# Kernel tuning notes

Measured on AMD Instinct MI355X. Metric: run time of the kernel, lower is better.

The kernel has to match this reference:

```python
import jax, jax.numpy as jnp
import numpy as np

B, N, C = 16, 4096, 512
FR = 2          # fr_ratio
NH = 8          # num_heads
CF = C // FR    # 256, q/k/v projection dim
HD = (C // NH) // FR  # 32, per-head dim after fr reduction
EPS = 1e-4


def _abs_clamp(t):
    # sign(t) * clamp(|t|, 1e-4, 1e4), as in the torch module's abs_clamp
    return jnp.sign(t) * jnp.clip(jnp.abs(t), 1e-4, 1e4)


def setup_inputs() -> dict:
    key = jax.random.key(0)
    ks = jax.random.split(key, 8)
    s = 0.02  # trunc_normal_(std=0.02) init scale
    return {
        "query": jax.random.normal(ks[0], (B, N, C), jnp.float32),
        "Wq": jax.random.normal(ks[1], (CF, C), jnp.float32) * s,
        "bq": jnp.zeros((CF,), jnp.float32),
        "Wk": jax.random.normal(ks[2], (CF, C), jnp.float32) * s,
        "bk": jnp.zeros((CF,), jnp.float32),
        "Wv": jax.random.normal(ks[3], (CF, C), jnp.float32) * s,
        "bv": jnp.zeros((CF,), jnp.float32),
        "Wo": jax.random.normal(ks[4], (C, CF), jnp.float32) * s,
        "bo": jnp.zeros((C,), jnp.float32),
        "Wse1": jax.random.normal(ks[5], (C // 2, C), jnp.float32) * s,
        "Wse2": jax.random.normal(ks[6], (C, C // 2), jnp.float32) * s,
        "H": 64,
        "W": 64,
    }


def reference(query, Wq, bq, Wk, bk, Wv, bv, Wo, bo, Wse1, Wse2, H, W):
    Bq, Nq, Cq = query.shape  # N == H*W
    # --- squeeze-excitation gate: mean over tokens -> 2-layer MLP -> sigmoid
    se = jnp.mean(query, axis=1)                                   # [B, C]
    se = jax.nn.sigmoid(jax.nn.relu(se @ Wse1.T) @ Wse2.T)         # [B, C]

    # --- q/k/v projections (sr_ratio=1: k/v from full-length query)
    q = jax.nn.relu(query @ Wq.T + bq).reshape(Bq, Nq, NH, HD)     # [B,N,h,d]
    k = jax.nn.relu(query @ Wk.T + bk).reshape(Bq, Nq, NH, HD)
    v = (query @ Wv.T + bv).reshape(Bq, Nq, NH, HD)

    # --- cosFormer-style 2D positional feature maps
    c = jnp.pi / 2
    idx = jnp.arange(Nq)
    a = (c * (idx // W).astype(query.dtype) / H)[None, :, None, None]  # row angle
    b = (c * (idx % W).astype(query.dtype) / W)[None, :, None, None]   # col angle
    q_ = jnp.concatenate([q * jnp.cos(a), q * jnp.sin(a),
                          q * jnp.cos(b), q * jnp.sin(b)], axis=-1)    # [B,N,h,4d]
    k_ = jnp.concatenate([k * jnp.cos(a), k * jnp.sin(a),
                          k * jnp.cos(b), k * jnp.sin(b)], axis=-1)    # sr_ratio=1 -> same angles

    # --- linear attention: kv state then q lookup, with abs-clamping
    kv = _abs_clamp(jnp.einsum('bnhf,bnhd->bhfd', k_, v))          # [B,h,4d,d]
    k_sum = jnp.sum(k_, axis=1, keepdims=True)                     # [B,1,h,4d]
    z = _abs_clamp(1.0 / (jnp.sum(q_ * k_sum, axis=-1) + EPS))     # [B,N,h]
    out = _abs_clamp(jnp.einsum('bnhf,bhfd->bnhd', q_, kv))        # [B,N,h,d]
    out = _abs_clamp(out * z[..., None])

    # --- output projection + SE residual gating
    out = _abs_clamp(out.reshape(Bq, Nq, CF) @ Wo.T + bo)          # [B,N,C]
    out = _abs_clamp(out + out * se[:, None, :])
    return out
```

## Files before the change

kernel.cpp:

```cpp
#include <hip/hip_runtime.h>
#include <math.h>

#define B_   16
#define N_   4096
#define C_   512
#define CF_  256
#define NH_  8
#define HD_  32
#define FHD_ 128
#define BN_  (B_ * N_)
#define EPS_ 1e-4f
#define PI2F 1.5707963267948966f

typedef _Float16 half8 __attribute__((ext_vector_type(8)));
typedef _Float16 half4 __attribute__((ext_vector_type(4)));
typedef _Float16 half2v __attribute__((ext_vector_type(2)));
typedef float f32x4 __attribute__((ext_vector_type(4)));
typedef unsigned short u16x8 __attribute__((ext_vector_type(8)));

__device__ __forceinline__ float abs_clamp(float t) {
    float a = fminf(fmaxf(fabsf(t), 1e-4f), 1e4f);
    return t > 0.f ? a : (t < 0.f ? -a : 0.f);
}
__device__ __forceinline__ void gld16(const void* g, void* l) {
    __builtin_amdgcn_global_load_lds(
        (const __attribute__((address_space(1))) void*)g,
        (__attribute__((address_space(3))) void*)l, 16, 0, 0);
}

__global__ __launch_bounds__(256) void se_sum_kernel(const float* __restrict__ q,
                                                     float* __restrict__ sesum,
                                                     _Float16* __restrict__ q16) {
    int b = blockIdx.x, chunk = blockIdx.y;
    int t = threadIdx.x;
    int c0 = 2 * t;
    const float* p = q + ((size_t)b * N_ + (size_t)chunk * 256) * C_ + c0;
    _Float16* o = q16 + ((size_t)b * N_ + (size_t)chunk * 256) * C_ + c0;
    float a0 = 0.f, a1 = 0.f;
    for (int n = 0; n < 256; n++) {
        float2 v = *(const float2*)(p + (size_t)n * C_);
        a0 += v.x;
        a1 += v.y;
        half2v hv;
        hv[0] = (_Float16)v.x;
        hv[1] = (_Float16)v.y;
        *(half2v*)(o + (size_t)n * C_) = hv;
    }
    atomicAdd(&sesum[b * C_ + c0], a0);
    atomicAdd(&sesum[b * C_ + c0 + 1], a1);
}

__global__ __launch_bounds__(256) void se_gate_kernel(const float* __restrict__ sesum,
                                                      const float* __restrict__ Wse1,
                                                      const float* __restrict__ Wse2,
                                                      float* __restrict__ segate) {
    __shared__ float sm[C_];
    __shared__ float hm[C_ / 2];
    int b = blockIdx.x, t = threadIdx.x;
    sm[t]       = sesum[b * C_ + t]       * (1.f / N_);
    sm[t + 256] = sesum[b * C_ + t + 256] * (1.f / N_);
    __syncthreads();
    {
        const float* w = Wse1 + (size_t)t * C_;
        float acc = 0.f;
        for (int c2 = 0; c2 < C_; c2++) acc += sm[c2] * w[c2];
        hm[t] = fmaxf(acc, 0.f);
    }
    __syncthreads();
    for (int r = 0; r < 2; r++) {
        int c2 = t + r * 256;
        const float* w2 = Wse2 + (size_t)c2 * (C_ / 2);
        float a2 = 0.f;
        for (int j = 0; j < C_ / 2; j++) a2 += hm[j] * w2[j];
        segate[b * C_ + c2] = 1.f / (1.f + expf(-a2));
    }
}

__global__ __launch_bounds__(256) void convert_w(const float* __restrict__ Wq,
                                                 const float* __restrict__ Wk,
                                                 const float* __restrict__ Wv,
                                                 const float* __restrict__ Wo,
                                                 _Float16* __restrict__ wcat,
                                                 _Float16* __restrict__ wo16) {
    int i = blockIdx.x * 256 + threadIdx.x;
    if (i < 768 * 512) {
        int r = i >> 9, c = i & 511;
        float w = (r < 256) ? Wq[(size_t)r * 512 + c]
                : (r < 512) ? Wk[(size_t)(r - 256) * 512 + c]
                            : Wv[(size_t)(r - 512) * 512 + c];
        wcat[i] = (_Float16)w;
    } else {
        int j = i - 768 * 512;
        wo16[j] = (_Float16)Wo[j];
    }
}

__global__ __launch_bounds__(256) void gemm_qkv(
    const _Float16* __restrict__ A16, const _Float16* __restrict__ Bw,
    const float* __restrict__ bq, const float* __restrict__ bk, const float* __restrict__ bv,
    _Float16* __restrict__ Oq, _Float16* __restrict__ kT, _Float16* __restrict__ vT) {
    constexpr int K = 512;
    constexpr int NITER = K / 32;

    __shared__ __align__(16) unsigned short As[2][128 * 32];
    __shared__ __align__(16) unsigned short Bs[2][128 * 32];

    const int t = threadIdx.x;
    const int did = blockIdx.x + 6 * blockIdx.y;
    const int lid = (did & 7) * 384 + (did >> 3);
    const int bx = lid % 6;
    const int Mb = (lid / 6) * 128;
    const int nrow0 = bx * 128;

    const int lane = t & 63;
    const int wv = t >> 6;
    const int mq = (wv >> 1) * 64;
    const int nq = (wv & 1) * 64;
    const int mrow = lane & 15;
    const int kq = lane >> 4;
    const int fragoff = mrow * 32 + ((kq ^ ((mrow >> 1) & 3)) * 8);

    const unsigned char *asrc0, *asrc1, *bsrc0, *bsrc1;
    int off0, off1;
    {
        int cid0 = t, cid1 = t + 256;
        int m0 = cid0 >> 2, c0 = (cid0 & 3) ^ ((m0 >> 1) & 3);
        int m1 = cid1 >> 2, c1 = (cid1 & 3) ^ ((m1 >> 1) & 3);
        asrc0 = (const unsigned char*)(A16 + (size_t)(Mb + m0) * K + c0 * 8);
        asrc1 = (const unsigned char*)(A16 + (size_t)(Mb + m1) * K + c1 * 8);
        bsrc0 = (const unsigned char*)(Bw + (size_t)(nrow0 + m0) * K + c0 * 8);
        bsrc1 = (const unsigned char*)(Bw + (size_t)(nrow0 + m1) * K + c1 * 8);
        off0 = cid0 * 8;
        off1 = cid1 * 8;
    }

    f32x4 acc[4][4];
#pragma unroll
    for (int mi = 0; mi < 4; mi++)
#pragma unroll
        for (int ni = 0; ni < 4; ni++) acc[mi][ni] = (f32x4){0.f, 0.f, 0.f, 0.f};

    gld16(asrc0, &As[0][off0]);
    gld16(asrc1, &As[0][off1]);
    gld16(bsrc0, &Bs[0][off0]);
    gld16(bsrc1, &Bs[0][off1]);
    __syncthreads();

    int cur = 0;
#pragma unroll 1
    for (int it = 0; it < NITER; ++it) {
        if (it + 1 < NITER) {
            gld16(asrc0 + (it + 1) * 64, &As[cur ^ 1][off0]);
            gld16(asrc1 + (it + 1) * 64, &As[cur ^ 1][off1]);
            gld16(bsrc0 + (it + 1) * 64, &Bs[cur ^ 1][off0]);
            gld16(bsrc1 + (it + 1) * 64, &Bs[cur ^ 1][off1]);
        }

        half8 ah[4], bh[4];
#pragma unroll
        for (int mi = 0; mi < 4; mi++)
            ah[mi] = *(const half8*)&As[cur][(mq + mi * 16) * 32 + fragoff];
#pragma unroll
        for (int ni = 0; ni < 4; ni++)
            bh[ni] = *(const half8*)&Bs[cur][(nq + ni * 16) * 32 + fragoff];
#pragma unroll
        for (int mi = 0; mi < 4; mi++)
#pragma unroll
            for (int ni = 0; ni < 4; ni++)
                acc[mi][ni] = __builtin_amdgcn_mfma_f32_16x16x32_f16(ah[mi], bh[ni], acc[mi][ni], 0, 0, 0);

        if (it + 1 < NITER) __syncthreads();
        cur ^= 1;
    }

#pragma unroll
    for (int ni = 0; ni < 4; ni++) {
        int gc = nrow0 + nq + ni * 16 + mrow;
        int mat = gc >> 8;
        int col = gc & 255;
        float bb = (mat == 0 ? bq : mat == 1 ? bk : bv)[col];
        if (mat == 0) {
#pragma unroll
            for (int mi = 0; mi < 4; mi++)
#pragma unroll
                for (int r = 0; r < 4; r++) {
                    int m = Mb + mq + mi * 16 + kq * 4 + r;
                    float v2 = fmaxf(acc[mi][ni][r] + bb, 0.f);
                    Oq[(size_t)m * CF_ + col] = (_Float16)v2;
                }
        } else {
            _Float16* OT = (mat == 1) ? kT : vT;
#pragma unroll
            for (int mi = 0; mi < 4; mi++) {
                int m0r = Mb + mq + mi * 16 + kq * 4;
                half4 hv;
#pragma unroll
                for (int r = 0; r < 4; r++) {
                    float v2 = acc[mi][ni][r] + bb;
                    if (mat == 1) v2 = fmaxf(v2, 0.f);
                    hv[r] = (_Float16)v2;
                }
                *(half4*)&OT[(size_t)col * BN_ + m0r] = hv;
            }
        }
    }
}

__global__ __launch_bounds__(256) void gemm_out(
    const _Float16* __restrict__ A16, const _Float16* __restrict__ Bw,
    const float* __restrict__ bo, const float* __restrict__ sg,
    float* __restrict__ Of) {
    constexpr int K = 256;
    constexpr int NITER = K / 32;

    __shared__ __align__(16) unsigned short As[2][128 * 32];
    __shared__ __align__(16) unsigned short Bs[2][128 * 32];

    const int t = threadIdx.x;
    const int did = blockIdx.x + 4 * blockIdx.y;
    const int lid = (did & 7) * 256 + (did >> 3);
    const int bx = lid & 3;
    const int Mb = (lid >> 2) * 128;
    const int nrow0 = bx * 128;

    const int lane = t & 63;
    const int wv = t >> 6;
    const int mq = (wv >> 1) * 64;
    const int nq = (wv & 1) * 64;
    const int mrow = lane & 15;
    const int kq = lane >> 4;
    const int fragoff = mrow * 32 + ((kq ^ ((mrow >> 1) & 3)) * 8);

    const unsigned char *asrc0, *asrc1, *bsrc0, *bsrc1;
    int off0, off1;
    {
        int cid0 = t, cid1 = t + 256;
        int m0 = cid0 >> 2, c0 = (cid0 & 3) ^ ((m0 >> 1) & 3);
        int m1 = cid1 >> 2, c1 = (cid1 & 3) ^ ((m1 >> 1) & 3);
        asrc0 = (const unsigned char*)(A16 + (size_t)(Mb + m0) * K + c0 * 8);
        asrc1 = (const unsigned char*)(A16 + (size_t)(Mb + m1) * K + c1 * 8);
        bsrc0 = (const unsigned char*)(Bw + (size_t)(nrow0 + m0) * K + c0 * 8);
        bsrc1 = (const unsigned char*)(Bw + (size_t)(nrow0 + m1) * K + c1 * 8);
        off0 = cid0 * 8;
        off1 = cid1 * 8;
    }

    f32x4 acc[4][4];
#pragma unroll
    for (int mi = 0; mi < 4; mi++)
#pragma unroll
        for (int ni = 0; ni < 4; ni++) acc[mi][ni] = (f32x4){0.f, 0.f, 0.f, 0.f};

    gld16(asrc0, &As[0][off0]);
    gld16(asrc1, &As[0][off1]);
    gld16(bsrc0, &Bs[0][off0]);
    gld16(bsrc1, &Bs[0][off1]);
    __syncthreads();

    int cur = 0;
#pragma unroll 1
    for (int it = 0; it < NITER; ++it) {
        if (it + 1 < NITER) {
            gld16(asrc0 + (it + 1) * 64, &As[cur ^ 1][off0]);
            gld16(asrc1 + (it + 1) * 64, &As[cur ^ 1][off1]);
            gld16(bsrc0 + (it + 1) * 64, &Bs[cur ^ 1][off0]);
            gld16(bsrc1 + (it + 1) * 64, &Bs[cur ^ 1][off1]);
        }

        half8 ah[4], bh[4];
#pragma unroll
        for (int mi = 0; mi < 4; mi++)
            ah[mi] = *(const half8*)&As[cur][(mq + mi * 16) * 32 + fragoff];
#pragma unroll
        for (int ni = 0; ni < 4; ni++)
            bh[ni] = *(const half8*)&Bs[cur][(nq + ni * 16) * 32 + fragoff];
#pragma unroll
        for (int mi = 0; mi < 4; mi++)
#pragma unroll
            for (int ni = 0; ni < 4; ni++)
                acc[mi][ni] = __builtin_amdgcn_mfma_f32_16x16x32_f16(ah[mi], bh[ni], acc[mi][ni], 0, 0, 0);

        if (it + 1 < NITER) __syncthreads();
        cur ^= 1;
    }

    int b = Mb >> 12;
#pragma unroll
    for (int ni = 0; ni < 4; ni++) {
        int gc = nrow0 + nq + ni * 16 + mrow;
        float bb = bo[gc];
        float gv = sg[b * C_ + gc];
#pragma unroll
        for (int mi = 0; mi < 4; mi++)
#pragma unroll
            for (int r = 0; r < 4; r++) {
                int m = Mb + mq + mi * 16 + kq * 4 + r;
                float v2 = abs_clamp(acc[mi][ni][r] + bb);
                v2 = abs_clamp(v2 * (1.f + gv));
                Of[(size_t)m * C_ + gc] = v2;
            }
    }
}

__global__ __launch_bounds__(256) void kv_mfma_kernel(const _Float16* __restrict__ kin,
                                                      const _Float16* __restrict__ vin,
                                                      float* __restrict__ kvout,
                                                      float* __restrict__ ksum) {
    __shared__ __align__(16) unsigned short Ah[128 * 64];
    __shared__ __align__(16) unsigned short Bh[48 * 64];

    const int t = threadIdx.x;
    const int c8 = blockIdx.x;
    const int h = blockIdx.y, b = blockIdx.z;
    const int dp = t & 31;
    const int octet = t >> 5;

    if (t < 128) {
        int r = 32 + (t & 15);
        int oc = t >> 4;
        int off = r * 64 + (((oc ^ ((r >> 3) & 7)) & 7) * 8);
        unsigned short fill = (r == 32) ? (unsigned short)0x3C00 : (unsigned short)0;
        u16x8 z = {fill, fill, fill, fill, fill, fill, fill, fill};
        *(u16x8*)&Bh[off] = z;
    }

    float cbv[8], sbv[8];
#pragma unroll
    for (int i = 0; i < 8; i++) {
        float ang = (PI2F / 64.f) * (float)(octet * 8 + i);
        cbv[i] = cosf(ang);
        sbv[i] = sinf(ang);
    }

    const int lane = t & 63;
    const int wv = t >> 6;
    const int mrow = lane & 15;
    const int kq = lane >> 4;

    f32x4 acc[2][3];
#pragma unroll
    for (int mi = 0; mi < 2; mi++)
#pragma unroll
        for (int ni = 0; ni < 3; ni++) acc[mi][ni] = (f32x4){0.f, 0.f, 0.f, 0.f};

    int offA[4];
#pragma unroll
    for (int tvar = 0; tvar < 4; tvar++) {
        int f = tvar * 32 + dp;
        offA[tvar] = f * 64 + (((octet ^ ((f >> 3) & 7)) & 7) * 8);
    }
    const int offB = dp * 64 + (((octet ^ ((dp >> 3) & 7)) & 7) * 8);

    const size_t colbase = (size_t)(h * HD_ + dp) * BN_ + (size_t)b * N_;

#pragma unroll 1
    for (int ch = 0; ch < 8; ch++) {
        const int n0 = c8 * 512 + ch * 64;
        const int rrow = n0 >> 6;
        float aang = (PI2F / 64.f) * (float)rrow;
        float ca = cosf(aang), sa = sinf(aang);

        half8 k8 = *(const half8*)(kin + colbase + n0 + octet * 8);
        half8 v8 = *(const half8*)(vin + colbase + n0 + octet * 8);
        float kvl[8];
#pragma unroll
        for (int i = 0; i < 8; i++) kvl[i] = (float)k8[i];

        __syncthreads();

#pragma unroll
        for (int tvar = 0; tvar < 4; tvar++) {
            half8 hv;
#pragma unroll
            for (int i = 0; i < 8; i++) {
                float val = kvl[i] * (tvar == 0 ? ca : tvar == 1 ? sa : tvar == 2 ? cbv[i] : sbv[i]);
                hv[i] = (_Float16)val;
            }
            *(half8*)&Ah[offA[tvar]] = hv;
        }
        *(half8*)&Bh[offB] = v8;
        __syncthreads();

#pragma unroll
        for (int s = 0; s < 2; s++) {
            half8 ah[2], bh[3];
            int koct = s * 4 + kq;
#pragma unroll
            for (int mi = 0; mi < 2; mi++) {
                int f = (wv * 2 + mi) * 16 + mrow;
                ah[mi] = *(const half8*)&Ah[f * 64 + (((koct ^ ((f >> 3) & 7)) & 7) * 8)];
            }
#pragma unroll
            for (int ni = 0; ni < 3; ni++) {
                int nr = ni * 16 + mrow;
                bh[ni] = *(const half8*)&Bh[nr * 64 + (((koct ^ ((nr >> 3) & 7)) & 7) * 8)];
            }
#pragma unroll
            for (int mi = 0; mi < 2; mi++)
#pragma unroll
                for (int ni = 0; ni < 3; ni++)
                    acc[mi][ni] = __builtin_amdgcn_mfma_f32_16x16x32_f16(ah[mi], bh[ni], acc[mi][ni], 0, 0, 0);
        }
    }

    float* kvp = kvout + (size_t)(b * NH_ + h) * FHD_ * HD_;
    float* ksp = ksum + (size_t)(b * NH_ + h) * FHD_;
#pragma unroll
    for (int mi = 0; mi < 2; mi++) {
        int mt = wv * 2 + mi;
#pragma unroll
        for (int r = 0; r < 4; r++) {
            int f = mt * 16 + kq * 4 + r;
            atomicAdd(&kvp[(size_t)mrow * FHD_ + f], acc[mi][0][r]);
            atomicAdd(&kvp[(size_t)(16 + mrow) * FHD_ + f], acc[mi][1][r]);
            if (mrow == 0) atomicAdd(&ksp[f], acc[mi][2][r]);
        }
    }
}

__global__ __launch_bounds__(256) void attn_kernel(const _Float16* __restrict__ qbuf,
                                                   const float* __restrict__ kvin,
                                                   const float* __restrict__ ksum,
                                                   _Float16* __restrict__ ob) {
    __shared__ __align__(16) unsigned short Aq[128 * 128];
    __shared__ __align__(16) unsigned short Bk[48 * 128];
    __shared__ float zS[128];

    const int chunk = blockIdx.x;
    const int h = blockIdx.y, b = blockIdx.z;
    const int t = threadIdx.x;
    const int n0 = chunk * 128;

    {
        const float* kvp = kvin + ((size_t)(b * NH_ + h)) * (HD_ * FHD_);
        int d = t >> 3;
        int c0 = (t & 7) * 2;
#pragma unroll
        for (int cc = 0; cc < 2; cc++) {
            int c = c0 + cc;
            const float* src = kvp + (size_t)d * FHD_ + c * 8;
            half8 hv;
#pragma unroll
            for (int i = 0; i < 8; i++) hv[i] = (_Float16)abs_clamp(src[i]);
            *(half8*)&Bk[d * 128 + ((c ^ (d & 7)) * 8)] = hv;
        }
        if (t < 16) {
            const float* ks = ksum + ((size_t)(b * NH_ + h)) * FHD_ + t * 8;
            half8 hv;
#pragma unroll
            for (int i = 0; i < 8; i++) hv[i] = (_Float16)ks[i];
            *(half8*)&Bk[32 * 128 + (t * 8)] = hv;
        } else {
            int idx = t - 16;
            int r = 33 + (idx >> 4), c = idx & 15;
            half8 z = {};
            *(half8*)&Bk[r * 128 + ((c ^ (r & 7)) * 8)] = z;
        }
    }
    {
        int tok = t >> 1, hf = t & 1;
        int n = n0 + tok;
        const _Float16* qp = qbuf + ((size_t)b * N_ + n) * CF_ + h * HD_;
        half8 q0 = *(const half8*)(qp + 0);
        half8 q1 = *(const half8*)(qp + 8);
        half8 q2 = *(const half8*)(qp + 16);
        half8 q3 = *(const half8*)(qp + 24);
        float f0, f1;
        if (hf == 0) {
            float aa = (PI2F / 64.f) * (float)(n >> 6);
            f0 = cosf(aa); f1 = sinf(aa);
        } else {
            float ab = (PI2F / 64.f) * (float)(n & 63);
            f0 = cosf(ab); f1 = sinf(ab);
        }
#pragma unroll
        for (int ti = 0; ti < 2; ti++) {
            float fac = ti ? f1 : f0;
#pragma unroll
            for (int dc = 0; dc < 4; dc++) {
                half8 qv = (dc == 0) ? q0 : (dc == 1) ? q1 : (dc == 2) ? q2 : q3;
                half8 hv;
#pragma unroll
                for (int i = 0; i < 8; i++) hv[i] = (_Float16)((float)qv[i] * fac);
                int c = hf * 8 + ti * 4 + dc;
                *(half8*)&Aq[tok * 128 + ((c ^ (tok & 7)) * 8)] = hv;
            }
        }
    }
    __syncthreads();

    const int lane = t & 63;
    const int wv = t >> 6;
    const int mrow = lane & 15;
    const int kq = lane >> 4;

    f32x4 acc[2][3];
#pragma unroll
    for (int mi = 0; mi < 2; mi++)
#pragma unroll
        for (int ni = 0; ni < 3; ni++) acc[mi][ni] = (f32x4){0.f, 0.f, 0.f, 0.f};

#pragma unroll
    for (int ks = 0; ks < 4; ks++) {
        half8 ah[2], bh[3];
        int cpos = ks * 4 + kq;
#pragma unroll
        for (int mi = 0; mi < 2; mi++) {
            int row = wv * 32 + mi * 16 + mrow;
            ah[mi] = *(const half8*)&Aq[row * 128 + ((cpos ^ (row & 7)) * 8)];
        }
#pragma unroll
        for (int ni = 0; ni < 3; ni++) {
            int row = ni * 16 + mrow;
            bh[ni] = *(const half8*)&Bk[row * 128 + ((cpos ^ (row & 7)) * 8)];
        }
#pragma unroll
        for (int mi = 0; mi < 2; mi++)
#pragma unroll
            for (int ni = 0; ni < 3; ni++)
                acc[mi][ni] = __builtin_amdgcn_mfma_f32_16x16x32_f16(ah[mi], bh[ni], acc[mi][ni], 0, 0, 0);
    }

    if (mrow == 0) {
#pragma unroll
        for (int mi = 0; mi < 2; mi++)
#pragma unroll
            for (int r = 0; r < 4; r++)
                zS[wv * 32 + mi * 16 + kq * 4 + r] = acc[mi][2][r];
    }
    __syncthreads();

#pragma unroll
    for (int mi = 0; mi < 2; mi++) {
#pragma unroll
        for (int r = 0; r < 4; r++) {
            int tok = wv * 32 + mi * 16 + kq * 4 + r;
            float z = abs_clamp(1.f / (zS[tok] + EPS_));
            float v0 = abs_clamp(abs_clamp(acc[mi][0][r]) * z);
            float v1 = abs_clamp(abs_clamp(acc[mi][1][r]) * z);
            size_t base = ((size_t)b * N_ + n0 + tok) * CF_ + h * HD_;
            ob[base + mrow] = (_Float16)v0;
            ob[base + 16 + mrow] = (_Float16)v1;
        }
    }
}

extern "C" void kernel_launch(void* const* d_in, const int* in_sizes, int n_in,
                              void* d_out, int out_size, void* d_ws, size_t ws_size,
                              hipStream_t stream) {
    (void)in_sizes; (void)n_in; (void)out_size; (void)ws_size;
    const float* query = (const float*)d_in[0];
    const float* Wq = (const float*)d_in[1];
    const float* bq = (const float*)d_in[2];
    const float* Wk = (const float*)d_in[3];
    const float* bk = (const float*)d_in[4];
    const float* Wv = (const float*)d_in[5];
    const float* bv = (const float*)d_in[6];
    const float* Wo = (const float*)d_in[7];
    const float* bo = (const float*)d_in[8];
    const float* Wse1 = (const float*)d_in[9];
    const float* Wse2 = (const float*)d_in[10];
    float* out = (float*)d_out;

    unsigned char* ws = (unsigned char*)d_ws;
    const size_t MB = 1024ull * 1024ull;
    _Float16* q16 = (_Float16*)(ws + 0);
    _Float16* ob  = (_Float16*)(ws + 0);
    _Float16* qb  = (_Float16*)(ws + 64 * MB);
    _Float16* kbT = (_Float16*)(ws + 96 * MB);
    _Float16* vbT = (_Float16*)(ws + 128 * MB);
    _Float16* wcat = (_Float16*)(ws + 160 * MB);
    _Float16* wo16 = (_Float16*)(ws + 160 * MB + 786432);
    float* kvb = (float*)(ws + 161 * MB);
    float* ksb = (float*)(ws + 163 * MB);
    float* ssb = (float*)(ws + 163 * MB + 65536);
    float* sgb = (float*)(ws + 163 * MB + 98304);

    hipMemsetAsync(kvb, 0, 2097152 + 65536 + 32768, stream);

    convert_w<<<2048, 256, 0, stream>>>(Wq, Wk, Wv, Wo, wcat, wo16);
    se_sum_kernel<<<dim3(B_, 16), 256, 0, stream>>>(query, ssb, q16);
    se_gate_kernel<<<B_, 256, 0, stream>>>(ssb, Wse1, Wse2, sgb);
    gemm_qkv<<<dim3(6, 512), 256, 0, stream>>>(q16, wcat, bq, bk, bv, qb, kbT, vbT);
    kv_mfma_kernel<<<dim3(8, NH_, B_), 256, 0, stream>>>(kbT, vbT, kvb, ksb);
    attn_kernel<<<dim3(32, NH_, B_), 256, 0, stream>>>(qb, kvb, ksb, ob);
    gemm_out<<<dim3(4, 512), 256, 0, stream>>>(ob, wo16, bo, sgb, out);
}
```

Measured before the change: 509.1 us.

## Restructure attention feature maps, widen kv chunks, and vectorize SE reduction

The SE sum/convert kernel now uses float4 loads over 32-token slices, and the grid is four times larger for more parallelism. The kv kernel processes 128 tokens per chunk with a wider LDS tile, halving the number of barrier iterations. The attention kernel stops building the 4x-expanded q feature map in LDS. It instead runs four MFMA passes of raw q against each kv block and combines them with per-token cos/sin factors. This cuts LDS writes and conversion work but increases the accumulator register count, which may reduce occupancy.

```diff
diff --git a/kernel.cpp b/kernel.cpp
--- a/kernel.cpp
+++ b/kernel.cpp
@@ -14,7 +14,6 @@
 
 typedef _Float16 half8 __attribute__((ext_vector_type(8)));
 typedef _Float16 half4 __attribute__((ext_vector_type(4)));
-typedef _Float16 half2v __attribute__((ext_vector_type(2)));
 typedef float f32x4 __attribute__((ext_vector_type(4)));
 typedef unsigned short u16x8 __attribute__((ext_vector_type(8)));
 
@@ -33,21 +32,24 @@
                                                      _Float16* __restrict__ q16) {
     int b = blockIdx.x, chunk = blockIdx.y;
     int t = threadIdx.x;
-    int c0 = 2 * t;
-    const float* p = q + ((size_t)b * N_ + (size_t)chunk * 256) * C_ + c0;
-    _Float16* o = q16 + ((size_t)b * N_ + (size_t)chunk * 256) * C_ + c0;
-    float a0 = 0.f, a1 = 0.f;
-    for (int n = 0; n < 256; n++) {
-        float2 v = *(const float2*)(p + (size_t)n * C_);
-        a0 += v.x;
-        a1 += v.y;
-        half2v hv;
-        hv[0] = (_Float16)v.x;
-        hv[1] = (_Float16)v.y;
-        *(half2v*)(o + (size_t)n * C_) = hv;
-    }
-    atomicAdd(&sesum[b * C_ + c0], a0);
-    atomicAdd(&sesum[b * C_ + c0 + 1], a1);
+    int c = (t & 127) * 4;
+    int tok0 = chunk * 64 + (t >> 7) * 32;
+    const float* p = q + ((size_t)b * N_ + tok0) * C_ + c;
+    _Float16* o = q16 + ((size_t)b * N_ + tok0) * C_ + c;
+    float a0 = 0.f, a1 = 0.f, a2 = 0.f, a3 = 0.f;
+#pragma unroll 4
+    for (int n = 0; n < 32; n++) {
+        float4 v = *(const float4*)(p + (size_t)n * C_);
+        a0 += v.x; a1 += v.y; a2 += v.z; a3 += v.w;
+        half4 hv;
+        hv[0] = (_Float16)v.x; hv[1] = (_Float16)v.y;
+        hv[2] = (_Float16)v.z; hv[3] = (_Float16)v.w;
+        *(half4*)(o + (size_t)n * C_) = hv;
+    }
+    atomicAdd(&sesum[b * C_ + c + 0], a0);
+    atomicAdd(&sesum[b * C_ + c + 1], a1);
+    atomicAdd(&sesum[b * C_ + c + 2], a2);
+    atomicAdd(&sesum[b * C_ + c + 3], a3);
 }
 
 __global__ __launch_bounds__(256) void se_gate_kernel(const float* __restrict__ sesum,
@@ -306,28 +308,27 @@
                                                       const _Float16* __restrict__ vin,
                                                       float* __restrict__ kvout,
                                                       float* __restrict__ ksum) {
-    __shared__ __align__(16) unsigned short Ah[128 * 64];
-    __shared__ __align__(16) unsigned short Bh[48 * 64];
+    __shared__ __align__(16) unsigned short Ah[128 * 128];
+    __shared__ __align__(16) unsigned short Bh[48 * 128];
 
     const int t = threadIdx.x;
     const int c8 = blockIdx.x;
     const int h = blockIdx.y, b = blockIdx.z;
     const int dp = t & 31;
-    const int octet = t >> 5;
-
-    if (t < 128) {
-        int r = 32 + (t & 15);
-        int oc = t >> 4;
-        int off = r * 64 + (((oc ^ ((r >> 3) & 7)) & 7) * 8);
+    const int oct = t >> 5;
+
+    {
+        int r = 32 + (t >> 4);
+        int c = t & 15;
         unsigned short fill = (r == 32) ? (unsigned short)0x3C00 : (unsigned short)0;
         u16x8 z = {fill, fill, fill, fill, fill, fill, fill, fill};
-        *(u16x8*)&Bh[off] = z;
+        *(u16x8*)&Bh[r * 128 + ((c ^ (r & 7)) * 8)] = z;
     }
 
     float cbv[8], sbv[8];
 #pragma unroll
     for (int i = 0; i < 8; i++) {
-        float ang = (PI2F / 64.f) * (float)(octet * 8 + i);
+        float ang = (PI2F / 64.f) * (float)(oct * 8 + i);
         cbv[i] = cosf(ang);
         sbv[i] = sinf(ang);
     }
@@ -343,57 +344,67 @@
 #pragma unroll
         for (int ni = 0; ni < 3; ni++) acc[mi][ni] = (f32x4){0.f, 0.f, 0.f, 0.f};
 
-    int offA[4];
+    int offAa[4], offAb[4];
 #pragma unroll
     for (int tvar = 0; tvar < 4; tvar++) {
         int f = tvar * 32 + dp;
-        offA[tvar] = f * 64 + (((octet ^ ((f >> 3) & 7)) & 7) * 8);
-    }
-    const int offB = dp * 64 + (((octet ^ ((dp >> 3) & 7)) & 7) * 8);
+        offAa[tvar] = f * 128 + ((oct ^ (f & 7)) * 8);
+        offAb[tvar] = f * 128 + (((oct + 8) ^ (f & 7)) * 8);
+    }
+    const int offBa = dp * 128 + ((oct ^ (dp & 7)) * 8);
+    const int offBb = dp * 128 + (((oct + 8) ^ (dp & 7)) * 8);
 
     const size_t colbase = (size_t)(h * HD_ + dp) * BN_ + (size_t)b * N_;
 
 #pragma unroll 1
-    for (int ch = 0; ch < 8; ch++) {
-        const int n0 = c8 * 512 + ch * 64;
-        const int rrow = n0 >> 6;
-        float aang = (PI2F / 64.f) * (float)rrow;
-        float ca = cosf(aang), sa = sinf(aang);
-
-        half8 k8 = *(const half8*)(kin + colbase + n0 + octet * 8);
-        half8 v8 = *(const half8*)(vin + colbase + n0 + octet * 8);
-        float kvl[8];
-#pragma unroll
-        for (int i = 0; i < 8; i++) kvl[i] = (float)k8[i];
+    for (int ch = 0; ch < 4; ch++) {
+        const int n0 = c8 * 512 + ch * 128;
+        const int rr = n0 >> 6;
+        float ca0 = cosf((PI2F / 64.f) * (float)rr),       sa0 = sinf((PI2F / 64.f) * (float)rr);
+        float ca1 = cosf((PI2F / 64.f) * (float)(rr + 1)), sa1 = sinf((PI2F / 64.f) * (float)(rr + 1));
+
+        const _Float16* kp = kin + colbase + n0 + oct * 8;
+        const _Float16* vp = vin + colbase + n0 + oct * 8;
+        half8 k8a = *(const half8*)kp;
+        half8 k8b = *(const half8*)(kp + 64);
+        half8 v8a = *(const half8*)vp;
+        half8 v8b = *(const half8*)(vp + 64);
+        float ka[8], kb[8];
+#pragma unroll
+        for (int i = 0; i < 8; i++) { ka[i] = (float)k8a[i]; kb[i] = (float)k8b[i]; }
 
         __syncthreads();
 
 #pragma unroll
         for (int tvar = 0; tvar < 4; tvar++) {
-            half8 hv;
+            half8 ha, hb;
 #pragma unroll
             for (int i = 0; i < 8; i++) {
-                float val = kvl[i] * (tvar == 0 ? ca : tvar == 1 ? sa : tvar == 2 ? cbv[i] : sbv[i]);
-                hv[i] = (_Float16)val;
+                float fa = (tvar == 0) ? ca0 : (tvar == 1) ? sa0 : (tvar == 2) ? cbv[i] : sbv[i];
+                float fb = (tvar == 0) ? ca1 : (tvar == 1) ? sa1 : (tvar == 2) ? cbv[i] : sbv[i];
+                ha[i] = (_Float16)(ka[i] * fa);
+                hb[i] = (_Float16)(kb[i] * fb);
             }
-            *(half8*)&Ah[offA[tvar]] = hv;
-        }
-        *(half8*)&Bh[offB] = v8;
+            *(half8*)&Ah[offAa[tvar]] = ha;
+            *(half8*)&Ah[offAb[tvar]] = hb;
+        }
+        *(half8*)&Bh[offBa] = v8a;
+        *(half8*)&Bh[offBb] = v8b;
         __syncthreads();
 
 #pragma unroll
-        for (int s = 0; s < 2; s++) {
+        for (int s = 0; s < 4; s++) {
+            int koct = s * 4 + kq;
             half8 ah[2], bh[3];
-            int koct = s * 4 + kq;
 #pragma unroll
             for (int mi = 0; mi < 2; mi++) {
                 int f = (wv * 2 + mi) * 16 + mrow;
-                ah[mi] = *(const half8*)&Ah[f * 64 + (((koct ^ ((f >> 3) & 7)) & 7) * 8)];
+                ah[mi] = *(const half8*)&Ah[f * 128 + ((koct ^ (f & 7)) * 8)];
             }
 #pragma unroll
             for (int ni = 0; ni < 3; ni++) {
                 int nr = ni * 16 + mrow;
-                bh[ni] = *(const half8*)&Bh[nr * 64 + (((koct ^ ((nr >> 3) & 7)) & 7) * 8)];
+                bh[ni] = *(const half8*)&Bh[nr * 128 + ((koct ^ (nr & 7)) * 8)];
             }
 #pragma unroll
             for (int mi = 0; mi < 2; mi++)
@@ -422,8 +433,9 @@
                                                    const float* __restrict__ kvin,
                                                    const float* __restrict__ ksum,
                                                    _Float16* __restrict__ ob) {
-    __shared__ __align__(16) unsigned short Aq[128 * 128];
+    __shared__ __align__(16) unsigned short Aq[128 * 40];
     __shared__ __align__(16) unsigned short Bk[48 * 128];
+    __shared__ __align__(16) float tS[128][4];
     __shared__ float zS[128];
 
     const int chunk = blockIdx.x;
@@ -459,33 +471,18 @@
     }
     {
         int tok = t >> 1, hf = t & 1;
-        int n = n0 + tok;
-        const _Float16* qp = qbuf + ((size_t)b * N_ + n) * CF_ + h * HD_;
-        half8 q0 = *(const half8*)(qp + 0);
-        half8 q1 = *(const half8*)(qp + 8);
-        half8 q2 = *(const half8*)(qp + 16);
-        half8 q3 = *(const half8*)(qp + 24);
-        float f0, f1;
-        if (hf == 0) {
-            float aa = (PI2F / 64.f) * (float)(n >> 6);
-            f0 = cosf(aa); f1 = sinf(aa);
-        } else {
-            float ab = (PI2F / 64.f) * (float)(n & 63);
-            f0 = cosf(ab); f1 = sinf(ab);
-        }
-#pragma unroll
-        for (int ti = 0; ti < 2; ti++) {
-            float fac = ti ? f1 : f0;
-#pragma unroll
-            for (int dc = 0; dc < 4; dc++) {
-                half8 qv = (dc == 0) ? q0 : (dc == 1) ? q1 : (dc == 2) ? q2 : q3;
-                half8 hv;
-#pragma unroll
-                for (int i = 0; i < 8; i++) hv[i] = (_Float16)((float)qv[i] * fac);
-                int c = hf * 8 + ti * 4 + dc;
-                *(half8*)&Aq[tok * 128 + ((c ^ (tok & 7)) * 8)] = hv;
-            }
-        }
+        const _Float16* qp = qbuf + ((size_t)b * N_ + n0 + tok) * CF_ + h * HD_ + hf * 16;
+        half8 a0 = *(const half8*)qp;
+        half8 a1 = *(const half8*)(qp + 8);
+        *(half8*)&Aq[tok * 40 + hf * 16] = a0;
+        *(half8*)&Aq[tok * 40 + hf * 16 + 8] = a1;
+    }
+    if (t < 128) {
+        int n = n0 + t;
+        float aa = (PI2F / 64.f) * (float)(n >> 6);
+        float ab = (PI2F / 64.f) * (float)(n & 63);
+        tS[t][0] = cosf(aa); tS[t][1] = sinf(aa);
+        tS[t][2] = cosf(ab); tS[t][3] = sinf(ab);
     }
     __syncthreads();
 
@@ -494,21 +491,23 @@
     const int mrow = lane & 15;
     const int kq = lane >> 4;
 
-    f32x4 acc[2][3];
+    half8 ah[2];
 #pragma unroll
     for (int mi = 0; mi < 2; mi++)
-#pragma unroll
-        for (int ni = 0; ni < 3; ni++) acc[mi][ni] = (f32x4){0.f, 0.f, 0.f, 0.f};
-
-#pragma unroll
-    for (int ks = 0; ks < 4; ks++) {
-        half8 ah[2], bh[3];
-        int cpos = ks * 4 + kq;
-#pragma unroll
-        for (int mi = 0; mi < 2; mi++) {
-            int row = wv * 32 + mi * 16 + mrow;
-            ah[mi] = *(const half8*)&Aq[row * 128 + ((cpos ^ (row & 7)) * 8)];
-        }
+        ah[mi] = *(const half8*)&Aq[(wv * 32 + mi * 16 + mrow) * 40 + kq * 8];
+
+    f32x4 acc[4][2][3];
+#pragma unroll
+    for (int tt = 0; tt < 4; tt++)
+#pragma unroll
+        for (int mi = 0; mi < 2; mi++)
+#pragma unroll
+            for (int ni = 0; ni < 3; ni++) acc[tt][mi][ni] = (f32x4){0.f, 0.f, 0.f, 0.f};
+
+#pragma unroll
+    for (int tt = 0; tt < 4; tt++) {
+        half8 bh[3];
+        int cpos = tt * 4 + kq;
 #pragma unroll
         for (int ni = 0; ni < 3; ni++) {
             int row = ni * 16 + mrow;
@@ -518,15 +517,20 @@
         for (int mi = 0; mi < 2; mi++)
 #pragma unroll
             for (int ni = 0; ni < 3; ni++)
-                acc[mi][ni] = __builtin_amdgcn_mfma_f32_16x16x32_f16(ah[mi], bh[ni], acc[mi][ni], 0, 0, 0);
+                acc[tt][mi][ni] = __builtin_amdgcn_mfma_f32_16x16x32_f16(ah[mi], bh[ni], acc[tt][mi][ni], 0, 0, 0);
     }
 
     if (mrow == 0) {
 #pragma unroll
         for (int mi = 0; mi < 2; mi++)
 #pragma unroll
-            for (int r = 0; r < 4; r++)
-                zS[wv * 32 + mi * 16 + kq * 4 + r] = acc[mi][2][r];
+            for (int r = 0; r < 4; r++) {
+                int tok = wv * 32 + mi * 16 + kq * 4 + r;
+                float4 tv = *(const float4*)&tS[tok][0];
+                float zraw = tv.x * acc[0][mi][2][r] + tv.y * acc[1][mi][2][r]
+                           + tv.z * acc[2][mi][2][r] + tv.w * acc[3][mi][2][r];
+                zS[tok] = abs_clamp(1.f / (zraw + EPS_));
+            }
     }
     __syncthreads();
 
@@ -535,9 +539,14 @@
 #pragma unroll
         for (int r = 0; r < 4; r++) {
             int tok = wv * 32 + mi * 16 + kq * 4 + r;
-            float z = abs_clamp(1.f / (zS[tok] + EPS_));
-            float v0 = abs_clamp(abs_clamp(acc[mi][0][r]) * z);
-            float v1 = abs_clamp(abs_clamp(acc[mi][1][r]) * z);
+            float4 tv = *(const float4*)&tS[tok][0];
+            float z = zS[tok];
+            float v0 = tv.x * acc[0][mi][0][r] + tv.y * acc[1][mi][0][r]
+                     + tv.z * acc[2][mi][0][r] + tv.w * acc[3][mi][0][r];
+            float v1 = tv.x * acc[0][mi][1][r] + tv.y * acc[1][mi][1][r]
+                     + tv.z * acc[2][mi][1][r] + tv.w * acc[3][mi][1][r];
+            v0 = abs_clamp(abs_clamp(v0) * z);
+            v1 = abs_clamp(abs_clamp(v1) * z);
             size_t base = ((size_t)b * N_ + n0 + tok) * CF_ + h * HD_;
             ob[base + mrow] = (_Float16)v0;
             ob[base + 16 + mrow] = (_Float16)v1;
@@ -579,7 +588,7 @@
     hipMemsetAsync(kvb, 0, 2097152 + 65536 + 32768, stream);
 
     convert_w<<<2048, 256, 0, stream>>>(Wq, Wk, Wv, Wo, wcat, wo16);
-    se_sum_kernel<<<dim3(B_, 16), 256, 0, stream>>>(query, ssb, q16);
+    se_sum_kernel<<<dim3(B_, 64), 256, 0, stream>>>(query, ssb, q16);
     se_gate_kernel<<<B_, 256, 0, stream>>>(ssb, Wse1, Wse2, sgb);
     gemm_qkv<<<dim3(6, 512), 256, 0, stream>>>(q16, wcat, bq, bk, bv, qb, kbT, vbT);
     kv_mfma_kernel<<<dim3(8, NH_, B_), 256, 0, stream>>>(kbT, vbT, kvb, ksb);
```

Measured after the change: 515.8 us. No clear change (+1.3%).
